# Kernel tuning notes

Hardware: AMD Instinct MI355X
Metric: run time of the kernel (lower is better)

Reference implementation:

```python
import jax, jax.numpy as jnp
import numpy as np

K = 8       # out_caps
H = 64      # nhidden
TAU = 1.0

def _l2norm(x, eps=1e-12):
    n = jnp.linalg.norm(x, axis=-1, keepdims=True)
    return x / jnp.maximum(n, eps)

def setup_inputs() -> dict:
    key = jax.random.key(0)
    k1, k2, k3, k4 = jax.random.split(key, 4)
    B, N, NB, D = 128, 50, 32, K * H
    return {
        "self_vectors": jax.random.normal(k1, (B, N, D), dtype=jnp.float32),
        "neighbor_vectors": jax.random.normal(k2, (B, N, NB, D), dtype=jnp.float32),
        "W1": jax.random.normal(k3, (D, D), dtype=jnp.float32) * 0.04,
        "b1": jax.random.normal(k4, (D,), dtype=jnp.float32) * 0.01,
        "max_iter": 3,
    }

def reference(self_vectors, neighbor_vectors, W1, b1, max_iter):
    B, N, _ = self_vectors.shape
    NB = neighbor_vectors.shape[2]
    # fc1 + ReLU projections (dropout p=0 -> identity)
    self_z = jax.nn.relu(self_vectors @ W1.T + b1)            # [B,N,K*H]
    neigh_z = jax.nn.relu(neighbor_vectors @ W1.T + b1)       # [B,N,NB,K*H]
    s = _l2norm(self_z.reshape(B, N, K, H))                   # [B,N,K,H]
    nz = _l2norm(neigh_z.reshape(B, N, NB, K, H))             # [B,N,NB,K,H]
    u = None
    for it in range(max_iter):
        if u is None:
            p = jnp.zeros((B, N, NB, K), dtype=s.dtype)
        else:
            p = jnp.einsum('bnmkh,bnkh->bnmk', nz, u)
        p = jax.nn.softmax(p / TAU, axis=-1)                   # softmax over K
        u = jnp.einsum('bnmkh,bnmk->bnkh', nz, p) + s          # sum over neighbors
        if it < max_iter - 1:
            u = _l2norm(u)
    return jax.nn.relu(u.reshape(B, N, K * H))
```

## Files before the change

### kernel.cpp

```cpp
#include <hip/hip_runtime.h>
#include <hip/hip_bf16.h>


#define D_DIM 512

typedef __attribute__((ext_vector_type(8))) short short8;
typedef __attribute__((ext_vector_type(4))) float f32x4;

static __device__ __forceinline__ short f2bf(float f) {
    __bf16 b = (__bf16)f;
    return __builtin_bit_cast(short, b);
}
static __device__ __forceinline__ float bf2f(short s) {
    unsigned u = ((unsigned)(unsigned short)s) << 16;
    return __builtin_bit_cast(float, u);
}
static __device__ __forceinline__ void gload_lds16(const void* g, void* l) {
    __builtin_amdgcn_global_load_lds(
        (const __attribute__((address_space(1))) void*)g,
        (__attribute__((address_space(3))) void*)l, 16, 0, 0);
}

__global__ __launch_bounds__(256) void wconv(const float* __restrict__ W,
                                             short* __restrict__ Wb) {
    const int i = (blockIdx.x * 256 + threadIdx.x) * 8;
    const float4 v0 = *reinterpret_cast<const float4*>(W + i);
    const float4 v1 = *reinterpret_cast<const float4*>(W + i + 4);
    short8 o;
    o[0] = f2bf(v0.x); o[1] = f2bf(v0.y); o[2] = f2bf(v0.z); o[3] = f2bf(v0.w);
    o[4] = f2bf(v1.x); o[5] = f2bf(v1.y); o[6] = f2bf(v1.z); o[7] = f2bf(v1.w);
    *reinterpret_cast<short8*>(Wb + i) = o;
}

__global__ __launch_bounds__(256, 2) void gemm_mfma(
    const float* __restrict__ A,
    const short* __restrict__ Wb,
    const float* __restrict__ bias,
    short* __restrict__ Z)
{
    __shared__ short lA[64 * 64];
    __shared__ short lB[512 * 64];

    const int t = threadIdx.x;
    const int lane = t & 63;
    const int wid = t >> 6;
    const size_t row0 = (size_t)blockIdx.x * 64;
    const int wc = wid * 128;

    const int arow0 = t >> 3;
    const int agcol = (t & 7) ^ (arow0 & 7);
    float4 ra[4];

    auto loadA = [&](int k0) {
        const float* p0 = A + (row0 + arow0) * D_DIM + k0 + agcol * 8;
        const float* p1 = A + (row0 + arow0 + 32) * D_DIM + k0 + agcol * 8;
        ra[0] = *reinterpret_cast<const float4*>(p0);
        ra[1] = *reinterpret_cast<const float4*>(p0 + 4);
        ra[2] = *reinterpret_cast<const float4*>(p1);
        ra[3] = *reinterpret_cast<const float4*>(p1 + 4);
    };
    auto writeA = [&]() {
        short8 c0, c1;
        c0[0] = f2bf(ra[0].x); c0[1] = f2bf(ra[0].y); c0[2] = f2bf(ra[0].z); c0[3] = f2bf(ra[0].w);
        c0[4] = f2bf(ra[1].x); c0[5] = f2bf(ra[1].y); c0[6] = f2bf(ra[1].z); c0[7] = f2bf(ra[1].w);
        c1[0] = f2bf(ra[2].x); c1[1] = f2bf(ra[2].y); c1[2] = f2bf(ra[2].z); c1[3] = f2bf(ra[2].w);
        c1[4] = f2bf(ra[3].x); c1[5] = f2bf(ra[3].y); c1[6] = f2bf(ra[3].z); c1[7] = f2bf(ra[3].w);
        *reinterpret_cast<short8*>(lA + t * 8) = c0;
        *reinterpret_cast<short8*>(lA + (t + 256) * 8) = c1;
    };
    auto stageB = [&](int k0) {
        #pragma unroll
        for (int i = 0; i < 16; ++i) {
            const int c = wid * 16 + i;
            const int brow = c * 8 + (lane >> 3);
            const int g = (lane & 7) ^ (brow & 7);
            gload_lds16(Wb + (size_t)brow * D_DIM + k0 + g * 8, lB + c * 512);
        }
    };

    f32x4 acc[4][8] = {};

    auto compute = [&]() {
        #pragma unroll
        for (int kh = 0; kh < 2; ++kh) {
            const int slot = kh * 4 + (lane >> 4);
            short8 af[4], bfr[8];
            #pragma unroll
            for (int m = 0; m < 4; ++m) {
                const int arow = m * 16 + (lane & 15);
                af[m] = *reinterpret_cast<const short8*>(
                    lA + arow * 64 + ((slot ^ (arow & 7)) * 8));
            }
            #pragma unroll
            for (int n = 0; n < 8; ++n) {
                const int brow = wc + n * 16 + (lane & 15);
                bfr[n] = *reinterpret_cast<const short8*>(
                    lB + brow * 64 + ((slot ^ (brow & 7)) * 8));
            }
            #pragma unroll
            for (int m = 0; m < 4; ++m)
                #pragma unroll
                for (int n = 0; n < 8; ++n)
                    acc[m][n] = __builtin_amdgcn_mfma_f32_16x16x32_bf16(
                        af[m], bfr[n], acc[m][n], 0, 0, 0);
        }
    };

    loadA(0);
    for (int tk = 0; tk < 8; ++tk) {
        writeA();
        stageB(tk * 64);
        if (tk < 7) loadA((tk + 1) * 64);
        __syncthreads();
        compute();
        if (tk < 7) __syncthreads();
    }

    const int cb = wc + (lane & 15);
    float bcol[8];
    #pragma unroll
    for (int n = 0; n < 8; ++n) bcol[n] = bias[cb + n * 16];

    #pragma unroll
    for (int m = 0; m < 4; ++m) {
        #pragma unroll
        for (int r = 0; r < 4; ++r) {
            float v[8];
            float ssa = 0.0f, ssb = 0.0f;
            #pragma unroll
            for (int n = 0; n < 4; ++n) {
                v[n] = fmaxf(acc[m][n][r] + bcol[n], 0.0f);
                ssa = fmaf(v[n], v[n], ssa);
            }
            #pragma unroll
            for (int n = 4; n < 8; ++n) {
                v[n] = fmaxf(acc[m][n][r] + bcol[n], 0.0f);
                ssb = fmaf(v[n], v[n], ssb);
            }
            ssa += __shfl_xor(ssa, 1); ssb += __shfl_xor(ssb, 1);
            ssa += __shfl_xor(ssa, 2); ssb += __shfl_xor(ssb, 2);
            ssa += __shfl_xor(ssa, 4); ssb += __shfl_xor(ssb, 4);
            ssa += __shfl_xor(ssa, 8); ssb += __shfl_xor(ssb, 8);
            const float inva = 1.0f / fmaxf(sqrtf(ssa), 1e-12f);
            const float invb = 1.0f / fmaxf(sqrtf(ssb), 1e-12f);
            const size_t orow = row0 + m * 16 + (lane >> 4) * 4 + r;
            #pragma unroll
            for (int n = 0; n < 4; ++n)
                Z[orow * D_DIM + cb + n * 16] = f2bf(v[n] * inva);
            #pragma unroll
            for (int n = 4; n < 8; ++n)
                Z[orow * D_DIM + cb + n * 16] = f2bf(v[n] * invb);
        }
    }
}

__global__ __launch_bounds__(256, 2) void routing_iters(
    const short* __restrict__ NZ,
    const short* __restrict__ S,
    const int* __restrict__ miter_ptr,
    float* __restrict__ out)
{
    __shared__ __align__(16) float nz[32 * 512];
    __shared__ __align__(16) float u[512];
    __shared__ float p[256];

    const int site = blockIdx.x;
    const int t = threadIdx.x;
    const int lane = t & 63;

    const short8* src = reinterpret_cast<const short8*>(NZ + (size_t)site * 32 * D_DIM);
    #pragma unroll
    for (int i = 0; i < 8; ++i) {
        const short8 c = src[t + 256 * i];
        const int base = (t + 256 * i) * 8;
        float4 f0, f1;
        f0.x = bf2f(c[0]); f0.y = bf2f(c[1]); f0.z = bf2f(c[2]); f0.w = bf2f(c[3]);
        f1.x = bf2f(c[4]); f1.y = bf2f(c[5]); f1.z = bf2f(c[6]); f1.w = bf2f(c[7]);
        *reinterpret_cast<float4*>(nz + base) = f0;
        *reinterpret_cast<float4*>(nz + base + 4) = f1;
    }

    const int e = 2 * t;
    const int kg = t >> 5;
    const short2 sv = *reinterpret_cast<const short2*>(S + (size_t)site * D_DIM + e);
    const float s0 = bf2f(sv.x), s1 = bf2f(sv.y);
    const int miter = *miter_ptr;

    __syncthreads();

    float a0 = 0.0f, a1 = 0.0f;
    for (int m = 0; m < 32; ++m) {
        const float2 z = *reinterpret_cast<const float2*>(nz + m * D_DIM + e);
        a0 += z.x; a1 += z.y;
    }
    float v0 = fmaf(a0, 0.125f, s0);
    float v1 = fmaf(a1, 0.125f, s1);

    const int m_ = t >> 3;
    const int k_ = t & 7;

    for (int it = 1; it < miter; ++it) {
        float ss = fmaf(v0, v0, v1 * v1);
        #pragma unroll
        for (int off = 16; off >= 1; off >>= 1) ss += __shfl_xor(ss, off);
        const float inv = 1.0f / fmaxf(sqrtf(ss), 1e-12f);
        v0 *= inv; v1 *= inv;
        *reinterpret_cast<float2*>(u + e) = make_float2(v0, v1);
        __syncthreads();

        const float4* nz4 = reinterpret_cast<const float4*>(nz + m_ * D_DIM + k_ * 64);
        const float4* u4  = reinterpret_cast<const float4*>(u + k_ * 64);
        float dot = 0.0f;
        #pragma unroll
        for (int i = 0; i < 16; ++i) {
            const int hh = (i + lane) & 15;
            const float4 a = nz4[hh];
            const float4 b = u4[hh];
            dot += a.x * b.x + a.y * b.y + a.z * b.z + a.w * b.w;
        }
        float mx = dot;
        mx = fmaxf(mx, __shfl_xor(mx, 1));
        mx = fmaxf(mx, __shfl_xor(mx, 2));
        mx = fmaxf(mx, __shfl_xor(mx, 4));
        const float pe = __expf(dot - mx);
        float psum = pe;
        psum += __shfl_xor(psum, 1);
        psum += __shfl_xor(psum, 2);
        psum += __shfl_xor(psum, 4);
        p[t] = pe / psum;
        __syncthreads();

        a0 = 0.0f; a1 = 0.0f;
        for (int m = 0; m < 32; ++m) {
            const float2 z = *reinterpret_cast<const float2*>(nz + m * D_DIM + e);
            const float pm = p[m * 8 + kg];
            a0 = fmaf(z.x, pm, a0);
            a1 = fmaf(z.y, pm, a1);
        }
        v0 = s0 + a0;
        v1 = s1 + a1;
        __syncthreads();
    }

    float2 o = make_float2(fmaxf(v0, 0.0f), fmaxf(v1, 0.0f));
    *reinterpret_cast<float2*>(out + (size_t)site * D_DIM + e) = o;
}

extern "C" void kernel_launch(void* const* d_in, const int* in_sizes, int n_in,
                              void* d_out, int out_size, void* d_ws, size_t ws_size,
                              hipStream_t stream) {
    const float* self_v  = (const float*)d_in[0];
    const float* neigh_v = (const float*)d_in[1];
    const float* W1      = (const float*)d_in[2];
    const float* b1      = (const float*)d_in[3];
    const int*   miter   = (const int*)d_in[4];
    float* out = (float*)d_out;

    const int sites = in_sizes[0] / D_DIM;
    const int nrows = in_sizes[1] / D_DIM;

    short* nz = (short*)d_ws;
    short* s  = nz + (size_t)nrows * D_DIM;
    short* Wb = s + (size_t)sites * D_DIM;

    wconv<<<dim3(D_DIM * D_DIM / (256 * 8)), dim3(256), 0, stream>>>(W1, Wb);
    gemm_mfma<<<dim3(nrows / 64), dim3(256), 0, stream>>>(neigh_v, Wb, b1, nz);
    gemm_mfma<<<dim3(sites / 64), dim3(256), 0, stream>>>(self_v, Wb, b1, s);
    routing_iters<<<dim3(sites), dim3(256), 0, stream>>>(nz, s, miter, out);
}
```

Before: 307.3 us.

## Fuse neighbor GEMM with routing iterations, keep normalized projections in LDS

The neighbor projection GEMM and the routing loop are merged into one kernel. Each 64-row block covers two sites and keeps its normalized bf16 projections in shared memory, so the routing phase reads them from there instead of from a global intermediate buffer. The GEMM main loop moves to a K-step of 32 with double-buffered LDS and a different swizzle, prefetching the next tile while the current one computes. The cost is 72KB of LDS per block, which may limit occupancy, and an extra barrier-heavy routing tail attached to each GEMM block.

```diff
diff --git a/kernel.cpp b/kernel.cpp
--- a/kernel.cpp
+++ b/kernel.cpp
@@ -3,8 +3,12 @@
 
 
 #define D_DIM 512
+#define BM 64
+#define BK 32
+#define KSTEPS (D_DIM / BK)
 
 typedef __attribute__((ext_vector_type(8))) short short8;
+typedef __attribute__((ext_vector_type(4))) short short4v;
 typedef __attribute__((ext_vector_type(4))) float f32x4;
 
 static __device__ __forceinline__ short f2bf(float f) {
@@ -32,90 +36,96 @@
     *reinterpret_cast<short8*>(Wb + i) = o;
 }
 
-__global__ __launch_bounds__(256, 2) void gemm_mfma(
+template <bool FUSED>
+__global__ __launch_bounds__(256, 2) void gemm_route(
     const float* __restrict__ A,
     const short* __restrict__ Wb,
     const float* __restrict__ bias,
-    short* __restrict__ Z)
+    short* __restrict__ Zs,
+    const short* __restrict__ S,
+    const int* __restrict__ miter_ptr,
+    float* __restrict__ out)
 {
-    __shared__ short lA[64 * 64];
-    __shared__ short lB[512 * 64];
+    __shared__ __align__(16) char smem[73728];
+    short* const lA = (short*)smem;
+    short* const lB = (short*)(smem + 8192);
 
     const int t = threadIdx.x;
     const int lane = t & 63;
     const int wid = t >> 6;
-    const size_t row0 = (size_t)blockIdx.x * 64;
+    const size_t row0 = (size_t)blockIdx.x * BM;
     const int wc = wid * 128;
 
-    const int arow0 = t >> 3;
-    const int agcol = (t & 7) ^ (arow0 & 7);
-    float4 ra[4];
-
-    auto loadA = [&](int k0) {
-        const float* p0 = A + (row0 + arow0) * D_DIM + k0 + agcol * 8;
-        const float* p1 = A + (row0 + arow0 + 32) * D_DIM + k0 + agcol * 8;
-        ra[0] = *reinterpret_cast<const float4*>(p0);
-        ra[1] = *reinterpret_cast<const float4*>(p0 + 4);
-        ra[2] = *reinterpret_cast<const float4*>(p1);
-        ra[3] = *reinterpret_cast<const float4*>(p1 + 4);
-    };
-    auto writeA = [&]() {
-        short8 c0, c1;
-        c0[0] = f2bf(ra[0].x); c0[1] = f2bf(ra[0].y); c0[2] = f2bf(ra[0].z); c0[3] = f2bf(ra[0].w);
-        c0[4] = f2bf(ra[1].x); c0[5] = f2bf(ra[1].y); c0[6] = f2bf(ra[1].z); c0[7] = f2bf(ra[1].w);
-        c1[0] = f2bf(ra[2].x); c1[1] = f2bf(ra[2].y); c1[2] = f2bf(ra[2].z); c1[3] = f2bf(ra[2].w);
-        c1[4] = f2bf(ra[3].x); c1[5] = f2bf(ra[3].y); c1[6] = f2bf(ra[3].z); c1[7] = f2bf(ra[3].w);
-        *reinterpret_cast<short8*>(lA + t * 8) = c0;
-        *reinterpret_cast<short8*>(lA + (t + 256) * 8) = c1;
-    };
-    auto stageB = [&](int k0) {
-        #pragma unroll
-        for (int i = 0; i < 16; ++i) {
-            const int c = wid * 16 + i;
-            const int brow = c * 8 + (lane >> 3);
-            const int g = (lane & 7) ^ (brow & 7);
-            gload_lds16(Wb + (size_t)brow * D_DIM + k0 + g * 8, lB + c * 512);
+    const int ar = t >> 2;
+    const int ap = t & 3;
+    const int ag = (ap - (ar >> 1)) & 3;
+    const float* const aPtr = A + (row0 + ar) * D_DIM + ag * 8;
+
+    float4 ra0, ra1;
+    auto loadAreg = [&](int k0) {
+        ra0 = *reinterpret_cast<const float4*>(aPtr + k0);
+        ra1 = *reinterpret_cast<const float4*>(aPtr + k0 + 4);
+    };
+    auto writeA = [&](int buf) {
+        short8 c;
+        c[0] = f2bf(ra0.x); c[1] = f2bf(ra0.y); c[2] = f2bf(ra0.z); c[3] = f2bf(ra0.w);
+        c[4] = f2bf(ra1.x); c[5] = f2bf(ra1.y); c[6] = f2bf(ra1.z); c[7] = f2bf(ra1.w);
+        *reinterpret_cast<short8*>(lA + buf * 2048 + ar * 32 + ap * 8) = c;
+    };
+    auto stageB = [&](int k0, int buf) {
+        #pragma unroll
+        for (int i = 0; i < 8; ++i) {
+            const int c = wid * 8 + i;
+            const int r = c * 16 + (lane >> 2);
+            const int p = lane & 3;
+            const int g = (p - (r >> 1)) & 3;
+            gload_lds16(Wb + (size_t)r * D_DIM + k0 + g * 8,
+                        lB + buf * 16384 + c * 512);
         }
     };
 
     f32x4 acc[4][8] = {};
 
-    auto compute = [&]() {
-        #pragma unroll
-        for (int kh = 0; kh < 2; ++kh) {
-            const int slot = kh * 4 + (lane >> 4);
-            short8 af[4], bfr[8];
-            #pragma unroll
-            for (int m = 0; m < 4; ++m) {
-                const int arow = m * 16 + (lane & 15);
-                af[m] = *reinterpret_cast<const short8*>(
-                    lA + arow * 64 + ((slot ^ (arow & 7)) * 8));
-            }
-            #pragma unroll
-            for (int n = 0; n < 8; ++n) {
-                const int brow = wc + n * 16 + (lane & 15);
-                bfr[n] = *reinterpret_cast<const short8*>(
-                    lB + brow * 64 + ((slot ^ (brow & 7)) * 8));
-            }
-            #pragma unroll
-            for (int m = 0; m < 4; ++m)
-                #pragma unroll
-                for (int n = 0; n < 8; ++n)
-                    acc[m][n] = __builtin_amdgcn_mfma_f32_16x16x32_bf16(
-                        af[m], bfr[n], acc[m][n], 0, 0, 0);
-        }
-    };
-
-    loadA(0);
-    for (int tk = 0; tk < 8; ++tk) {
-        writeA();
-        stageB(tk * 64);
-        if (tk < 7) loadA((tk + 1) * 64);
+    auto compute = [&](int buf) {
+        const int s_ = lane >> 4;
+        short8 af[4], bfr[8];
+        #pragma unroll
+        for (int m = 0; m < 4; ++m) {
+            const int r = m * 16 + (lane & 15);
+            af[m] = *reinterpret_cast<const short8*>(
+                lA + buf * 2048 + r * 32 + ((s_ + (r >> 1)) & 3) * 8);
+        }
+        #pragma unroll
+        for (int n = 0; n < 8; ++n) {
+            const int r = wc + n * 16 + (lane & 15);
+            bfr[n] = *reinterpret_cast<const short8*>(
+                lB + buf * 16384 + r * 32 + ((s_ + (r >> 1)) & 3) * 8);
+        }
+        #pragma unroll
+        for (int m = 0; m < 4; ++m)
+            #pragma unroll
+            for (int n = 0; n < 8; ++n)
+                acc[m][n] = __builtin_amdgcn_mfma_f32_16x16x32_bf16(
+                    af[m], bfr[n], acc[m][n], 0, 0, 0);
+    };
+
+    loadAreg(0);
+    stageB(0, 0);
+    writeA(0);
+    __syncthreads();
+    int cur = 0;
+    for (int tk = 0; tk < KSTEPS; ++tk) {
+        if (tk < KSTEPS - 1) {
+            loadAreg((tk + 1) * BK);
+            stageB((tk + 1) * BK, cur ^ 1);
+        }
+        compute(cur);
+        if (tk < KSTEPS - 1) writeA(cur ^ 1);
         __syncthreads();
-        compute();
-        if (tk < 7) __syncthreads();
-    }
-
+        cur ^= 1;
+    }
+
+    short* const zbuf = (short*)(smem + 8192);
     const int cb = wc + (lane & 15);
     float bcol[8];
     #pragma unroll
@@ -143,107 +153,110 @@
             ssa += __shfl_xor(ssa, 8); ssb += __shfl_xor(ssb, 8);
             const float inva = 1.0f / fmaxf(sqrtf(ssa), 1e-12f);
             const float invb = 1.0f / fmaxf(sqrtf(ssb), 1e-12f);
-            const size_t orow = row0 + m * 16 + (lane >> 4) * 4 + r;
-            #pragma unroll
-            for (int n = 0; n < 4; ++n)
-                Z[orow * D_DIM + cb + n * 16] = f2bf(v[n] * inva);
-            #pragma unroll
-            for (int n = 4; n < 8; ++n)
-                Z[orow * D_DIM + cb + n * 16] = f2bf(v[n] * invb);
-        }
-    }
-}
-
-__global__ __launch_bounds__(256, 2) void routing_iters(
-    const short* __restrict__ NZ,
-    const short* __restrict__ S,
-    const int* __restrict__ miter_ptr,
-    float* __restrict__ out)
-{
-    __shared__ __align__(16) float nz[32 * 512];
-    __shared__ __align__(16) float u[512];
-    __shared__ float p[256];
-
-    const int site = blockIdx.x;
-    const int t = threadIdx.x;
-    const int lane = t & 63;
-
-    const short8* src = reinterpret_cast<const short8*>(NZ + (size_t)site * 32 * D_DIM);
-    #pragma unroll
-    for (int i = 0; i < 8; ++i) {
-        const short8 c = src[t + 256 * i];
-        const int base = (t + 256 * i) * 8;
-        float4 f0, f1;
-        f0.x = bf2f(c[0]); f0.y = bf2f(c[1]); f0.z = bf2f(c[2]); f0.w = bf2f(c[3]);
-        f1.x = bf2f(c[4]); f1.y = bf2f(c[5]); f1.z = bf2f(c[6]); f1.w = bf2f(c[7]);
-        *reinterpret_cast<float4*>(nz + base) = f0;
-        *reinterpret_cast<float4*>(nz + base + 4) = f1;
-    }
-
-    const int e = 2 * t;
-    const int kg = t >> 5;
-    const short2 sv = *reinterpret_cast<const short2*>(S + (size_t)site * D_DIM + e);
-    const float s0 = bf2f(sv.x), s1 = bf2f(sv.y);
+            const int orow = m * 16 + (lane >> 4) * 4 + r;
+            if (FUSED) {
+                #pragma unroll
+                for (int n = 0; n < 4; ++n)
+                    zbuf[orow * D_DIM + cb + n * 16] = f2bf(v[n] * inva);
+                #pragma unroll
+                for (int n = 4; n < 8; ++n)
+                    zbuf[orow * D_DIM + cb + n * 16] = f2bf(v[n] * invb);
+            } else {
+                #pragma unroll
+                for (int n = 0; n < 4; ++n)
+                    Zs[(row0 + orow) * D_DIM + cb + n * 16] = f2bf(v[n] * inva);
+                #pragma unroll
+                for (int n = 4; n < 8; ++n)
+                    Zs[(row0 + orow) * D_DIM + cb + n * 16] = f2bf(v[n] * invb);
+            }
+        }
+    }
+
+    if (!FUSED) return;
+    __syncthreads();
+
+    float* const scratch = (float*)smem;
+    const int tt = t & 127;
+    const int ssid = t >> 7;
+    const size_t site = (size_t)blockIdx.x * 2 + ssid;
+    float* const u  = scratch + ssid * 512;
+    float* const pp = scratch + 1024 + ssid * 256;
+    const short* const zr = zbuf + ssid * 32 * D_DIM;
+
+    const int e = tt * 4;
+    const int go = tt >> 4;
+    const short4v sv = *reinterpret_cast<const short4v*>(S + site * D_DIM + e);
+    const float s0 = bf2f(sv[0]), s1 = bf2f(sv[1]), s2 = bf2f(sv[2]), s3 = bf2f(sv[3]);
     const int miter = *miter_ptr;
 
-    __syncthreads();
-
-    float a0 = 0.0f, a1 = 0.0f;
-    for (int m = 0; m < 32; ++m) {
-        const float2 z = *reinterpret_cast<const float2*>(nz + m * D_DIM + e);
-        a0 += z.x; a1 += z.y;
-    }
-    float v0 = fmaf(a0, 0.125f, s0);
-    float v1 = fmaf(a1, 0.125f, s1);
-
-    const int m_ = t >> 3;
-    const int k_ = t & 7;
+    float v0, v1, v2, v3;
+    {
+        float a0 = 0, a1 = 0, a2 = 0, a3 = 0;
+        for (int m = 0; m < 32; ++m) {
+            const short4v z = *reinterpret_cast<const short4v*>(zr + m * D_DIM + e);
+            a0 += bf2f(z[0]); a1 += bf2f(z[1]); a2 += bf2f(z[2]); a3 += bf2f(z[3]);
+        }
+        v0 = fmaf(a0, 0.125f, s0); v1 = fmaf(a1, 0.125f, s1);
+        v2 = fmaf(a2, 0.125f, s2); v3 = fmaf(a3, 0.125f, s3);
+    }
+
+    const int dm = tt >> 2;
+    const int ka = (tt & 3) * 2;
 
     for (int it = 1; it < miter; ++it) {
-        float ss = fmaf(v0, v0, v1 * v1);
-        #pragma unroll
-        for (int off = 16; off >= 1; off >>= 1) ss += __shfl_xor(ss, off);
-        const float inv = 1.0f / fmaxf(sqrtf(ss), 1e-12f);
-        v0 *= inv; v1 *= inv;
-        *reinterpret_cast<float2*>(u + e) = make_float2(v0, v1);
+        float ssum = v0 * v0 + v1 * v1 + v2 * v2 + v3 * v3;
+        ssum += __shfl_xor(ssum, 1);
+        ssum += __shfl_xor(ssum, 2);
+        ssum += __shfl_xor(ssum, 4);
+        ssum += __shfl_xor(ssum, 8);
+        const float inv = 1.0f / fmaxf(sqrtf(ssum), 1e-12f);
+        v0 *= inv; v1 *= inv; v2 *= inv; v3 *= inv;
+        *reinterpret_cast<float4*>(u + e) = make_float4(v0, v1, v2, v3);
         __syncthreads();
 
-        const float4* nz4 = reinterpret_cast<const float4*>(nz + m_ * D_DIM + k_ * 64);
-        const float4* u4  = reinterpret_cast<const float4*>(u + k_ * 64);
-        float dot = 0.0f;
-        #pragma unroll
-        for (int i = 0; i < 16; ++i) {
-            const int hh = (i + lane) & 15;
-            const float4 a = nz4[hh];
-            const float4 b = u4[hh];
-            dot += a.x * b.x + a.y * b.y + a.z * b.z + a.w * b.w;
-        }
-        float mx = dot;
+        const short* const za = zr + dm * D_DIM + ka * 64;
+        const float* const ua = u + ka * 64;
+        float da = 0, db = 0;
+        #pragma unroll
+        for (int j = 0; j < 8; ++j) {
+            const int jj = ((j + (tt & 7)) & 7) * 8;
+            const short8 zva = *reinterpret_cast<const short8*>(za + jj);
+            const short8 zvb = *reinterpret_cast<const short8*>(za + 64 + jj);
+            const f32x4 uA0 = *reinterpret_cast<const f32x4*>(ua + jj);
+            const f32x4 uA1 = *reinterpret_cast<const f32x4*>(ua + jj + 4);
+            const f32x4 uB0 = *reinterpret_cast<const f32x4*>(ua + 64 + jj);
+            const f32x4 uB1 = *reinterpret_cast<const f32x4*>(ua + 64 + jj + 4);
+            #pragma unroll
+            for (int q = 0; q < 4; ++q) {
+                da = fmaf(bf2f(zva[q]), uA0[q], da);
+                da = fmaf(bf2f(zva[q + 4]), uA1[q], da);
+                db = fmaf(bf2f(zvb[q]), uB0[q], db);
+                db = fmaf(bf2f(zvb[q + 4]), uB1[q], db);
+            }
+        }
+        float mx = fmaxf(da, db);
         mx = fmaxf(mx, __shfl_xor(mx, 1));
         mx = fmaxf(mx, __shfl_xor(mx, 2));
-        mx = fmaxf(mx, __shfl_xor(mx, 4));
-        const float pe = __expf(dot - mx);
-        float psum = pe;
-        psum += __shfl_xor(psum, 1);
-        psum += __shfl_xor(psum, 2);
-        psum += __shfl_xor(psum, 4);
-        p[t] = pe / psum;
+        const float ea = __expf(da - mx), eb = __expf(db - mx);
+        float sm_ = ea + eb;
+        sm_ += __shfl_xor(sm_, 1);
+        sm_ += __shfl_xor(sm_, 2);
+        const float rs = 1.0f / sm_;
+        *reinterpret_cast<float2*>(pp + dm * 8 + ka) = make_float2(ea * rs, eb * rs);
         __syncthreads();
 
-        a0 = 0.0f; a1 = 0.0f;
+        float a0 = 0, a1 = 0, a2 = 0, a3 = 0;
         for (int m = 0; m < 32; ++m) {
-            const float2 z = *reinterpret_cast<const float2*>(nz + m * D_DIM + e);
-            const float pm = p[m * 8 + kg];
-            a0 = fmaf(z.x, pm, a0);
-            a1 = fmaf(z.y, pm, a1);
-        }
-        v0 = s0 + a0;
-        v1 = s1 + a1;
-        __syncthreads();
-    }
-
-    float2 o = make_float2(fmaxf(v0, 0.0f), fmaxf(v1, 0.0f));
-    *reinterpret_cast<float2*>(out + (size_t)site * D_DIM + e) = o;
+            const short4v z = *reinterpret_cast<const short4v*>(zr + m * D_DIM + e);
+            const float pm = pp[m * 8 + go];
+            a0 = fmaf(bf2f(z[0]), pm, a0); a1 = fmaf(bf2f(z[1]), pm, a1);
+            a2 = fmaf(bf2f(z[2]), pm, a2); a3 = fmaf(bf2f(z[3]), pm, a3);
+        }
+        v0 = s0 + a0; v1 = s1 + a1; v2 = s2 + a2; v3 = s3 + a3;
+    }
+
+    *reinterpret_cast<float4*>(out + site * D_DIM + e) =
+        make_float4(fmaxf(v0, 0.0f), fmaxf(v1, 0.0f), fmaxf(v2, 0.0f), fmaxf(v3, 0.0f));
 }
 
 extern "C" void kernel_launch(void* const* d_in, const int* in_sizes, int n_in,
@@ -259,12 +272,12 @@
     const int sites = in_sizes[0] / D_DIM;
     const int nrows = in_sizes[1] / D_DIM;
 
-    short* nz = (short*)d_ws;
-    short* s  = nz + (size_t)nrows * D_DIM;
+    short* s  = (short*)d_ws;
     short* Wb = s + (size_t)sites * D_DIM;
 
     wconv<<<dim3(D_DIM * D_DIM / (256 * 8)), dim3(256), 0, stream>>>(W1, Wb);
-    gemm_mfma<<<dim3(nrows / 64), dim3(256), 0, stream>>>(neigh_v, Wb, b1, nz);
-    gemm_mfma<<<dim3(sites / 64), dim3(256), 0, stream>>>(self_v, Wb, b1, s);
-    routing_iters<<<dim3(sites), dim3(256), 0, stream>>>(nz, s, miter, out);
-}
+    gemm_route<false><<<dim3(sites / BM), dim3(256), 0, stream>>>(
+        self_v, Wb, b1, s, nullptr, nullptr, nullptr);
+    gemm_route<true><<<dim3(nrows / BM), dim3(256), 0, stream>>>(
+        neigh_v, Wb, b1, nullptr, s, miter, out);
+}
```

Measured after the change: 283.8 us. 7.6% less time.
